# Performance work log

Hardware: AMD Instinct MI355X
Metric: run time of the kernel (lower is better)

Reference implementation:

```python
import jax, jax.numpy as jnp
import numpy as np
from jax import lax

B, C, CI, H, W_SP = 8, 64, 3, 224, 224  # batch, per-channel groups, in-chans per group, spatial
K, STRIDE = 5, 2


def setup_inputs() -> dict:
    key = jax.random.key(0)
    kx, kw = jax.random.split(key)
    x = jax.random.normal(kx, (B, C, CI, H, W_SP), dtype=jnp.float32)
    # one Conv2d(3->1, k=5, stride=2, bias=False) per output channel -> stacked [C, CI, K, K]
    fan_in = CI * K * K
    bound = 1.0 / np.sqrt(fan_in)
    W = jax.random.uniform(kw, (C, CI, K, K), dtype=jnp.float32, minval=-bound, maxval=bound)
    return {"x": x, "W": W}


def reference(x, W):
    # x: [B, C, CI, H, W]; each of the C groups has its own 3->1 conv (weights W[c]).
    # Equivalent to a single grouped conv: input [B, C*CI, H, W], feature_group_count=C.
    b, c, ci, h, w = x.shape
    x2 = x.reshape(b, c * ci, h, w)
    out = lax.conv_general_dilated(
        x2, W,
        window_strides=(STRIDE, STRIDE),
        padding="VALID",
        feature_group_count=c,
        dimension_numbers=("NCHW", "OIHW", "NCHW"),
    )  # [B, C, H_out, W_out]
    return out
```

## Files before the change

kernel.cpp:

```cpp
#include <hip/hip_runtime.h>

#define BATCH 8
#define CH 64
#define CIN 3
#define HIN 224
#define WIN 224
#define KSZ 5
#define STRIDE 2
#define HO 110
#define WO 110
#define RY 5
#define GROUPS (HO / RY)
#define ITEMS (GROUPS * WO)
#define BLOCKS_X ((ITEMS + 255) / 256)
#define NPLANES (BATCH * CH)
#define NWG (BLOCKS_X * NPLANES)
#define NROWS (2 * (RY - 1) + KSZ)

typedef float float4u __attribute__((ext_vector_type(4), aligned(8)));

__global__ __launch_bounds__(256) void conv5_reg_kernel(
    const float* __restrict__ x,
    const float* __restrict__ Wt,
    float* __restrict__ out)
{
    __shared__ float wsh[CIN * KSZ * KSZ];

    const int wg = blockIdx.x;
    const int per = NWG >> 3;
    const int swz = (wg & 7) * per + (wg >> 3);
    const int bc   = swz / BLOCKS_X;
    const int xblk = swz - bc * BLOCKS_X;
    const int c = bc & (CH - 1);

    const int tid = threadIdx.x;
    if (tid < CIN * KSZ * KSZ) {
        wsh[tid] = Wt[c * (CIN * KSZ * KSZ) + tid];
    }
    __syncthreads();

    const int idx = xblk * 256 + tid;
    if (idx >= ITEMS) return;

    const int wo  = idx % WO;
    const int g   = idx / WO;
    const int ho0 = g * RY;
    const int ih0 = ho0 * STRIDE;
    const int iw0 = wo * STRIDE;

    float acc[RY] = {0.f, 0.f, 0.f, 0.f, 0.f};

    const float* xb = x + (size_t)bc * (CIN * HIN * WIN);

#pragma unroll
    for (int ci = 0; ci < CIN; ++ci) {
        float wr[KSZ * KSZ];
#pragma unroll
        for (int i = 0; i < KSZ * KSZ; ++i) wr[i] = wsh[ci * KSZ * KSZ + i];

        const float* xp = xb + (size_t)ci * HIN * WIN + (size_t)ih0 * WIN + iw0;
#pragma unroll
        for (int r = 0; r < NROWS; ++r) {
            const float* rp = xp + r * WIN;
            float4u v4 = *reinterpret_cast<const float4u*>(rp);
            float   v5 = rp[4];
            float xv[KSZ] = {v4.x, v4.y, v4.z, v4.w, v5};
#pragma unroll
            for (int t = 0; t < RY; ++t) {
                const int kh = r - STRIDE * t;
                if (kh >= 0 && kh < KSZ) {
#pragma unroll
                    for (int kw = 0; kw < KSZ; ++kw) {
                        acc[t] = fmaf(xv[kw], wr[kh * KSZ + kw], acc[t]);
                    }
                }
            }
        }
    }

    float* op = out + (size_t)bc * (HO * WO) + (size_t)ho0 * WO + wo;
#pragma unroll
    for (int t = 0; t < RY; ++t) {
        op[t * WO] = acc[t];
    }
}

extern "C" void kernel_launch(void* const* d_in, const int* in_sizes, int n_in,
                              void* d_out, int out_size, void* d_ws, size_t ws_size,
                              hipStream_t stream)
{
    const float* x  = (const float*)d_in[0];
    const float* Wt = (const float*)d_in[1];
    float* out = (float*)d_out;

    conv5_reg_kernel<<<dim3(NWG), dim3(256), 0, stream>>>(x, Wt, out);
}
```

Measured before the change: 83.44 us.

## Enlarge per-thread register tile to 10 rows by 2 columns

Each thread now computes a 10x2 block of outputs instead of a 5x1 column. Every loaded input row feeds two adjacent output columns and a taller run of output rows. Inputs are read as two aligned float4 loads per row, and outputs are written as float2 stores. The aim is to cut redundant global and cache loads from overlapping windows and to raise FMA work per load, in exchange for more registers per thread, 128-thread blocks and some idle threads in the last block of each plane.

Measured after the change: 84.02 us. No clear change (+0.7%).

```diff
diff --git a/kernel.cpp b/kernel.cpp
--- a/kernel.cpp
+++ b/kernel.cpp
@@ -9,17 +9,22 @@
 #define STRIDE 2
 #define HO 110
 #define WO 110
-#define RY 5
+#define RY 10
+#define RX 2
 #define GROUPS (HO / RY)
-#define ITEMS (GROUPS * WO)
-#define BLOCKS_X ((ITEMS + 255) / 256)
+#define PAIRS (WO / RX)
+#define ITEMS (GROUPS * PAIRS)
+#define TPB 128
+#define BLOCKS_X ((ITEMS + TPB - 1) / TPB)
 #define NPLANES (BATCH * CH)
 #define NWG (BLOCKS_X * NPLANES)
-#define NROWS (2 * (RY - 1) + KSZ)
+#define NROWS (STRIDE * (RY - 1) + KSZ)
+#define RWIDTH (STRIDE * (RX - 1) + KSZ)
 
-typedef float float4u __attribute__((ext_vector_type(4), aligned(8)));
+typedef float float4a __attribute__((ext_vector_type(4)));
+typedef float float2a __attribute__((ext_vector_type(2)));
 
-__global__ __launch_bounds__(256) void conv5_reg_kernel(
+__global__ __launch_bounds__(TPB) void conv5_reg2_kernel(
     const float* __restrict__ x,
     const float* __restrict__ Wt,
     float* __restrict__ out)
@@ -39,16 +44,20 @@
     }
     __syncthreads();
 
-    const int idx = xblk * 256 + tid;
+    const int idx = xblk * TPB + tid;
     if (idx >= ITEMS) return;
 
-    const int wo  = idx % WO;
-    const int g   = idx / WO;
+    const int px = idx % PAIRS;
+    const int g  = idx / PAIRS;
     const int ho0 = g * RY;
     const int ih0 = ho0 * STRIDE;
-    const int iw0 = wo * STRIDE;
+    const int iw0 = px * (RX * STRIDE);
 
-    float acc[RY] = {0.f, 0.f, 0.f, 0.f, 0.f};
+    float acc[RY][RX];
+#pragma unroll
+    for (int t = 0; t < RY; ++t)
+#pragma unroll
+        for (int u = 0; u < RX; ++u) acc[t][u] = 0.f;
 
     const float* xb = x + (size_t)bc * (CIN * HIN * WIN);
 
@@ -62,26 +71,29 @@
 #pragma unroll
         for (int r = 0; r < NROWS; ++r) {
             const float* rp = xp + r * WIN;
-            float4u v4 = *reinterpret_cast<const float4u*>(rp);
-            float   v5 = rp[4];
-            float xv[KSZ] = {v4.x, v4.y, v4.z, v4.w, v5};
+            float4a v0 = *reinterpret_cast<const float4a*>(rp);
+            float4a v1 = *reinterpret_cast<const float4a*>(rp + 4);
+            float xv[8] = {v0.x, v0.y, v0.z, v0.w, v1.x, v1.y, v1.z, v1.w};
 #pragma unroll
             for (int t = 0; t < RY; ++t) {
                 const int kh = r - STRIDE * t;
                 if (kh >= 0 && kh < KSZ) {
 #pragma unroll
                     for (int kw = 0; kw < KSZ; ++kw) {
-                        acc[t] = fmaf(xv[kw], wr[kh * KSZ + kw], acc[t]);
+                        const float w = wr[kh * KSZ + kw];
+                        acc[t][0] = fmaf(xv[kw],     w, acc[t][0]);
+                        acc[t][1] = fmaf(xv[kw + 2], w, acc[t][1]);
                     }
                 }
             }
         }
     }
 
-    float* op = out + (size_t)bc * (HO * WO) + (size_t)ho0 * WO + wo;
+    float* op = out + (size_t)bc * (HO * WO) + (size_t)ho0 * WO + px * RX;
 #pragma unroll
     for (int t = 0; t < RY; ++t) {
-        op[t * WO] = acc[t];
+        float2a v = {acc[t][0], acc[t][1]};
+        *reinterpret_cast<float2a*>(op + (size_t)t * WO) = v;
     }
 }
 
@@ -93,5 +105,5 @@
     const float* Wt = (const float*)d_in[1];
     float* out = (float*)d_out;
 
-    conv5_reg_kernel<<<dim3(NWG), dim3(256), 0, stream>>>(x, Wt, out);
+    conv5_reg2_kernel<<<dim3(NWG), dim3(TPB), 0, stream>>>(x, Wt, out);
 }
```
